# Optimization experiments

Measured on AMD Instinct MI355X. Metric: run time of the kernel, lower is better.

Reference implementation:

```python
import jax, jax.numpy as jnp
import numpy as np
import math

BLOCK_SIZE = 128  # config.block_size


def setup_inputs() -> dict:
    key = jax.random.key(0)
    k1, k2, k3 = jax.random.split(key, 3)
    B, H, S, D = 2, 12, 4096, 64
    return {
        "query_layer": jax.random.normal(k1, (B, H, S, D), dtype=jnp.float32),
        "key_layer": jax.random.normal(k2, (B, H, S, D), dtype=jnp.float32),
        "value_layer": jax.random.normal(k3, (B, H, S, D), dtype=jnp.float32),
        "attention_mask": jnp.zeros((B, 1, 1, S), dtype=jnp.float32),
    }


def reference(query_layer, key_layer, value_layer, attention_mask):
    d = query_layer.shape[-1]
    # [B,H,S,S] attention scores
    scores = jnp.einsum("bhqd,bhkd->bhqk", query_layer, key_layer) / math.sqrt(d)
    scores = scores + attention_mask
    # Faithful to source: the bottom-right block is OVERWRITTEN with
    # tril(ones, -1).T * finfo.min  (0 on/below diag, min strictly above)
    bs = BLOCK_SIZE
    causal_mask = jnp.tril(jnp.ones((bs, bs), dtype=scores.dtype), k=-1).T
    causal_mask = causal_mask * jnp.finfo(scores.dtype).min
    scores = scores.at[..., -bs:, -bs:].set(causal_mask)
    probs = jax.nn.softmax(scores, axis=-1)
    # dropout is identity in eval mode
    return jnp.einsum("bhqk,bhkd->bhqd", probs, value_layer)
```

## Files before the change

kernel.cpp:

```cpp
#include <hip/hip_runtime.h>

#define S_LEN 4096
#define DH    64
#define BQ    128
#define BK    64
#define NTILE (S_LEN / BK)
#define QBLKS (S_LEN / BQ)
#define NBH   24
#define NHEADS 12

typedef __attribute__((ext_vector_type(8))) short short8;
typedef __attribute__((ext_vector_type(4))) short short4v;
typedef __attribute__((ext_vector_type(4))) float f32x4;

#define PSTR 72
#define KSTR 72
#define VSTR 72
#define LOG2E 1.44269504088896f
#define MCONST (-12.99718425f)

#define NKCH (NBH * S_LEN * DH / 8)

__device__ __forceinline__ short f2bf(float x) {
    unsigned u = __builtin_bit_cast(unsigned, x);
    return (short)((u + 0x8000u) >> 16);
}

typedef __attribute__((address_space(1))) const unsigned int guint;
typedef __attribute__((address_space(3))) unsigned int luint;
__device__ __forceinline__ void g2l16(const short* g, short* l) {
    __builtin_amdgcn_global_load_lds((guint*)g, (luint*)l, 16, 0, 0);
}

__global__ __launch_bounds__(256)
void prepass(const float* __restrict__ K, const float* __restrict__ V,
             const float* __restrict__ M, short* __restrict__ Kf,
             short* __restrict__ Vtf, float* __restrict__ Mf)
{
    __shared__ __align__(16) short K_lds[BK * KSTR];
    __shared__ __align__(16) short Vt_lds[DH * VSTR];

    const int tid = threadIdx.x;
    const int bh  = blockIdx.x >> 6;
    const int t   = blockIdx.x & 63;
    const size_t base = ((size_t)bh * S_LEN + (size_t)t * BK) * DH;

    #pragma unroll
    for (int it = 0; it < 4; ++it) {
        int idx = tid + 256 * it;
        int row = idx >> 4, c4 = idx & 15;
        float4 v = *(const float4*)(K + base + (size_t)row * DH + 4 * c4);
        short4v b4 = { f2bf(v.x), f2bf(v.y), f2bf(v.z), f2bf(v.w) };
        *(short4v*)&K_lds[row * KSTR + 4 * c4] = b4;
    }
    {
        int kb = tid >> 4, db = tid & 15;
        const float* vp = V + base + (size_t)(4 * kb) * DH + 4 * db;
        float4 r0 = *(const float4*)(vp);
        float4 r1 = *(const float4*)(vp + DH);
        float4 r2 = *(const float4*)(vp + 2 * DH);
        float4 r3 = *(const float4*)(vp + 3 * DH);
        short4v c0 = { f2bf(r0.x), f2bf(r1.x), f2bf(r2.x), f2bf(r3.x) };
        short4v c1 = { f2bf(r0.y), f2bf(r1.y), f2bf(r2.y), f2bf(r3.y) };
        short4v c2 = { f2bf(r0.z), f2bf(r1.z), f2bf(r2.z), f2bf(r3.z) };
        short4v c3 = { f2bf(r0.w), f2bf(r1.w), f2bf(r2.w), f2bf(r3.w) };
        *(short4v*)&Vt_lds[(4 * db + 0) * VSTR + 4 * kb] = c0;
        *(short4v*)&Vt_lds[(4 * db + 1) * VSTR + 4 * kb] = c1;
        *(short4v*)&Vt_lds[(4 * db + 2) * VSTR + 4 * kb] = c2;
        *(short4v*)&Vt_lds[(4 * db + 3) * VSTR + 4 * kb] = c3;
    }
    __syncthreads();

    const size_t obase = (size_t)(bh * NTILE + t) * 4096;
    #pragma unroll
    for (int e = 0; e < 2; ++e) {
        int ci = tid + 256 * e;
        int lane = ci & 63, n = lane & 15, q = lane >> 4;
        {
            int kt = (ci >> 6) & 1, mt = ci >> 7;
            short8 f = *(const short8*)&K_lds[(16 * mt + n) * KSTR + 32 * kt + 8 * q];
            *(short8*)&Kf[obase + (size_t)ci * 8] = f;
        }
        {
            int d = (ci >> 6) & 3, kt2 = (ci >> 8) & 1;
            short8 g2 = *(const short8*)&Vt_lds[(16 * d + n) * VSTR + 32 * kt2 + 8 * q];
            *(short8*)&Vtf[obase + (size_t)ci * 8] = g2;
        }
    }
    if ((bh % NHEADS) == 0 && tid < 16) {
        int b_idx = bh / NHEADS;
        float4 mv = *(const float4*)(M + (size_t)b_idx * S_LEN + t * BK + 4 * tid);
        mv.x = mv.x * LOG2E + MCONST;
        mv.y = mv.y * LOG2E + MCONST;
        mv.z = mv.z * LOG2E + MCONST;
        mv.w = mv.w * LOG2E + MCONST;
        *(float4*)&Mf[(size_t)b_idx * S_LEN + t * BK + 4 * tid] = mv;
    }
}

__global__ __launch_bounds__(256, 3)
void fa6(const float* __restrict__ Q, const short* __restrict__ Kf,
         const short* __restrict__ Vtf, const float* __restrict__ Mf,
         float* __restrict__ O)
{
    __shared__ __align__(16) short Ks[2][4096];
    __shared__ __align__(16) short Vs[2][4096];
    __shared__ __align__(16) short P_lds[BQ * PSTR];

    const int tid  = threadIdx.x;
    const int w    = tid >> 6;
    const int lane = tid & 63;
    const int n    = lane & 15;
    const int quad = lane >> 4;

    const int bid  = blockIdx.x;
    const int x    = bid & 7;
    const int g    = bid >> 3;
    const int bh   = x + 8 * (g >> 5);
    const int qblk = g & 31;
    const bool special = (qblk == QBLKS - 1);

    const size_t base  = (size_t)bh * S_LEN * DH;
    const int    b_idx = bh / NHEADS;

    const float QSCALE = 0.125f * LOG2E;
    const int q0 = qblk * BQ + w * 32;
    short8 qf[2][2];
    #pragma unroll
    for (int s = 0; s < 2; ++s) {
        const float* qp = Q + base + (size_t)(q0 + 16 * s + n) * DH;
        #pragma unroll
        for (int kt = 0; kt < 2; ++kt) {
            const float* p = qp + 32 * kt + 8 * quad;
            float4 a = *(const float4*)p;
            float4 b = *(const float4*)(p + 4);
            short8 f;
            f[0] = f2bf(a.x * QSCALE); f[1] = f2bf(a.y * QSCALE);
            f[2] = f2bf(a.z * QSCALE); f[3] = f2bf(a.w * QSCALE);
            f[4] = f2bf(b.x * QSCALE); f[5] = f2bf(b.y * QSCALE);
            f[6] = f2bf(b.z * QSCALE); f[7] = f2bf(b.w * QSCALE);
            qf[s][kt] = f;
        }
    }

    f32x4 o[4][2];
    #pragma unroll
    for (int d = 0; d < 4; ++d)
        #pragma unroll
        for (int s = 0; s < 2; ++s) o[d][s] = (f32x4){0.f, 0.f, 0.f, 0.f};
    f32x4 lsum[2] = { (f32x4){0.f,0.f,0.f,0.f}, (f32x4){0.f,0.f,0.f,0.f} };

    const short8 ONES = { 0x3F80, 0x3F80, 0x3F80, 0x3F80,
                          0x3F80, 0x3F80, 0x3F80, 0x3F80 };
    const float* mrow = Mf + (size_t)b_idx * S_LEN;
    const short* Kg = Kf  + (size_t)(bh * NTILE) * 4096;
    const short* Vg = Vtf + (size_t)(bh * NTILE) * 4096;

    #pragma unroll
    for (int i = 0; i < 2; ++i) {
        int c = 2 * w + i;
        g2l16(Kg + c * 512 + lane * 8, &Ks[0][c * 512]);
        g2l16(Vg + c * 512 + lane * 8, &Vs[0][c * 512]);
    }
    __syncthreads();

    for (int t = 0; t < NTILE; ++t) {
        const bool sp = special && t >= NTILE - 2;
        const int  cur = t & 1, nxt = cur ^ 1;

        {
            int tn = (t + 1 < NTILE) ? t + 1 : t;
            const short* kg = Kg + (size_t)tn * 4096;
            const short* vg = Vg + (size_t)tn * 4096;
            #pragma unroll
            for (int i = 0; i < 2; ++i) {
                int c = 2 * w + i;
                g2l16(kg + c * 512 + lane * 8, &Ks[nxt][c * 512]);
                g2l16(vg + c * 512 + lane * 8, &Vs[nxt][c * 512]);
            }
        }

        if (!sp) {
            f32x4 acc[4][2];
            #pragma unroll
            for (int mt = 0; mt < 4; ++mt) {
                short8 k0 = *(const short8*)&Ks[cur][(2 * mt    ) * 512 + lane * 8];
                short8 k1 = *(const short8*)&Ks[cur][(2 * mt + 1) * 512 + lane * 8];
                f32x4 mk = *(const f32x4*)(mrow + t * BK + 16 * mt + 4 * quad);
                #pragma unroll
                for (int s = 0; s < 2; ++s) {
                    f32x4 c = mk;
                    c = __builtin_amdgcn_mfma_f32_16x16x32_bf16(k0, qf[s][0], c, 0, 0, 0);
                    c = __builtin_amdgcn_mfma_f32_16x16x32_bf16(k1, qf[s][1], c, 0, 0, 0);
                    acc[mt][s] = c;
                }
            }
            #pragma unroll
            for (int s = 0; s < 2; ++s) {
                int qrow = w * 32 + 16 * s + n;
                #pragma unroll
                for (int mt = 0; mt < 4; ++mt) {
                    float p0 = __builtin_amdgcn_exp2f(acc[mt][s][0]);
                    float p1 = __builtin_amdgcn_exp2f(acc[mt][s][1]);
                    float p2 = __builtin_amdgcn_exp2f(acc[mt][s][2]);
                    float p3 = __builtin_amdgcn_exp2f(acc[mt][s][3]);
                    unsigned d0 = __builtin_amdgcn_perm(
                        __builtin_bit_cast(unsigned, p1),
                        __builtin_bit_cast(unsigned, p0), 0x07060302u);
                    unsigned d1 = __builtin_amdgcn_perm(
                        __builtin_bit_cast(unsigned, p3),
                        __builtin_bit_cast(unsigned, p2), 0x07060302u);
                    *(uint2*)&P_lds[qrow * PSTR + 16 * mt + 4 * quad] = make_uint2(d0, d1);
                }
            }
        } else {
            #pragma unroll
            for (int s = 0; s < 2; ++s) {
                int ql2 = w * 32 + 16 * s + n;
                #pragma unroll
                for (int mt = 0; mt < 4; ++mt) {
                    int k0 = (t - (NTILE - 2)) * BK + 16 * mt + 4 * quad;
                    unsigned d0 = (k0     > ql2 ? 0u : 0x3900u)
                                | (k0 + 1 > ql2 ? 0u : 0x39000000u);
                    unsigned d1 = (k0 + 2 > ql2 ? 0u : 0x3900u)
                                | (k0 + 3 > ql2 ? 0u : 0x39000000u);
                    *(uint2*)&P_lds[ql2 * PSTR + 16 * mt + 4 * quad] = make_uint2(d0, d1);
                }
            }
        }

        #pragma unroll
        for (int kt2 = 0; kt2 < 2; ++kt2) {
            short8 pf0 = *(const short8*)&P_lds[(w * 32 + n) * PSTR + 32 * kt2 + 8 * quad];
            short8 pf1 = *(const short8*)&P_lds[(w * 32 + 16 + n) * PSTR + 32 * kt2 + 8 * quad];
            lsum[0] = __builtin_amdgcn_mfma_f32_16x16x32_bf16(ONES, pf0, lsum[0], 0, 0, 0);
            lsum[1] = __builtin_amdgcn_mfma_f32_16x16x32_bf16(ONES, pf1, lsum[1], 0, 0, 0);
            #pragma unroll
            for (int d = 0; d < 4; ++d) {
                short8 vf = *(const short8*)&Vs[cur][(kt2 * 4 + d) * 512 + lane * 8];
                o[d][0] = __builtin_amdgcn_mfma_f32_16x16x32_bf16(vf, pf0, o[d][0], 0, 0, 0);
                o[d][1] = __builtin_amdgcn_mfma_f32_16x16x32_bf16(vf, pf1, o[d][1], 0, 0, 0);
            }
        }

        __syncthreads();
    }

    #pragma unroll
    for (int s = 0; s < 2; ++s) {
        float inv = 1.0f / lsum[s][0];
        int qg = q0 + 16 * s + n;
        float* op = O + base + (size_t)qg * DH;
        #pragma unroll
        for (int d = 0; d < 4; ++d) {
            f32x4 r = o[d][s] * inv;
            *(f32x4*)(op + 16 * d + 4 * quad) = r;
        }
    }
}

extern "C" void kernel_launch(void* const* d_in, const int* in_sizes, int n_in,
                              void* d_out, int out_size, void* d_ws, size_t ws_size,
                              hipStream_t stream) {
    const float* Q = (const float*)d_in[0];
    const float* K = (const float*)d_in[1];
    const float* V = (const float*)d_in[2];
    const float* M = (const float*)d_in[3];
    float* O = (float*)d_out;

    short* Kf  = (short*)d_ws;
    short* Vtf = Kf + (size_t)NKCH * 8;
    float* Mf  = (float*)(Vtf + (size_t)NKCH * 8);

    prepass<<<dim3(NBH * NTILE), dim3(256), 0, stream>>>(K, V, M, Kf, Vtf, Mf);
    fa6<<<dim3(NBH * QBLKS), dim3(256), 0, stream>>>(Q, Kf, Vtf, Mf, O);
}
```

Baseline: 228.8 us.

## Load V fragments directly to registers and use per-wave P layout

V tiles are no longer staged through double-buffered LDS. Each lane now loads its V MFMA fragments from global memory straight into registers at the start of every tile. The P scratch is reorganised into a per-wave layout with 16-byte writes and a permuted read pattern, and the special causal tile now builds P directly in registers instead of writing it to LDS. This cuts LDS footprint and traffic, but adds global-load latency to every tile that is not prefetched ahead and raises register pressure.

```diff
diff --git a/kernel.cpp b/kernel.cpp
--- a/kernel.cpp
+++ b/kernel.cpp
@@ -12,13 +12,18 @@
 typedef __attribute__((ext_vector_type(8))) short short8;
 typedef __attribute__((ext_vector_type(4))) short short4v;
 typedef __attribute__((ext_vector_type(4))) float f32x4;
-
-#define PSTR 72
+typedef __attribute__((ext_vector_type(4))) unsigned uint4v;
+
 #define KSTR 72
 #define VSTR 72
 #define LOG2E 1.44269504088896f
 #define MCONST (-12.99718425f)
 
+#define P_MT    8
+#define P_NSTR  48
+#define P_QSTR  784
+#define P_SSTR  (4 * P_QSTR)
+#define P_WAVE  (2 * P_SSTR)
 #define NKCH (NBH * S_LEN * DH / 8)
 
 __device__ __forceinline__ short f2bf(float x) {
@@ -99,13 +104,12 @@
 }
 
 __global__ __launch_bounds__(256, 3)
-void fa6(const float* __restrict__ Q, const short* __restrict__ Kf,
+void fa7(const float* __restrict__ Q, const short* __restrict__ Kf,
          const short* __restrict__ Vtf, const float* __restrict__ Mf,
          float* __restrict__ O)
 {
     __shared__ __align__(16) short Ks[2][4096];
-    __shared__ __align__(16) short Vs[2][4096];
-    __shared__ __align__(16) short P_lds[BQ * PSTR];
+    __shared__ __align__(16) char  P_s[4 * P_WAVE];
 
     const int tid  = threadIdx.x;
     const int w    = tid >> 6;
@@ -154,13 +158,13 @@
                           0x3F80, 0x3F80, 0x3F80, 0x3F80 };
     const float* mrow = Mf + (size_t)b_idx * S_LEN;
     const short* Kg = Kf  + (size_t)(bh * NTILE) * 4096;
-    const short* Vg = Vtf + (size_t)(bh * NTILE) * 4096;
+    const short* Vg = Vtf + (size_t)(bh * NTILE) * 4096 + (size_t)lane * 8;
+    char* Pw = &P_s[w * P_WAVE];
 
     #pragma unroll
     for (int i = 0; i < 2; ++i) {
         int c = 2 * w + i;
         g2l16(Kg + c * 512 + lane * 8, &Ks[0][c * 512]);
-        g2l16(Vg + c * 512 + lane * 8, &Vs[0][c * 512]);
     }
     __syncthreads();
 
@@ -168,15 +172,20 @@
         const bool sp = special && t >= NTILE - 2;
         const int  cur = t & 1, nxt = cur ^ 1;
 
+        short8 vfr[8];
+        {
+            const short* vb = Vg + (size_t)t * 4096;
+            #pragma unroll
+            for (int i = 0; i < 8; ++i) vfr[i] = *(const short8*)(vb + i * 512);
+        }
+
         {
             int tn = (t + 1 < NTILE) ? t + 1 : t;
             const short* kg = Kg + (size_t)tn * 4096;
-            const short* vg = Vg + (size_t)tn * 4096;
             #pragma unroll
             for (int i = 0; i < 2; ++i) {
                 int c = 2 * w + i;
                 g2l16(kg + c * 512 + lane * 8, &Ks[nxt][c * 512]);
-                g2l16(vg + c * 512 + lane * 8, &Vs[nxt][c * 512]);
             }
         }
 
@@ -197,49 +206,53 @@
             }
             #pragma unroll
             for (int s = 0; s < 2; ++s) {
-                int qrow = w * 32 + 16 * s + n;
+                unsigned dd0[4], dd1[4];
                 #pragma unroll
                 for (int mt = 0; mt < 4; ++mt) {
                     float p0 = __builtin_amdgcn_exp2f(acc[mt][s][0]);
                     float p1 = __builtin_amdgcn_exp2f(acc[mt][s][1]);
                     float p2 = __builtin_amdgcn_exp2f(acc[mt][s][2]);
                     float p3 = __builtin_amdgcn_exp2f(acc[mt][s][3]);
-                    unsigned d0 = __builtin_amdgcn_perm(
+                    dd0[mt] = __builtin_amdgcn_perm(
                         __builtin_bit_cast(unsigned, p1),
                         __builtin_bit_cast(unsigned, p0), 0x07060302u);
-                    unsigned d1 = __builtin_amdgcn_perm(
+                    dd1[mt] = __builtin_amdgcn_perm(
                         __builtin_bit_cast(unsigned, p3),
                         __builtin_bit_cast(unsigned, p2), 0x07060302u);
-                    *(uint2*)&P_lds[qrow * PSTR + 16 * mt + 4 * quad] = make_uint2(d0, d1);
                 }
-            }
-        } else {
+                char* pw = Pw + s * P_SSTR + quad * P_QSTR + n * P_NSTR;
+                uint4v w0 = { dd0[0], dd1[0], dd0[1], dd1[1] };
+                uint4v w1 = { dd0[2], dd1[2], dd0[3], dd1[3] };
+                *(uint4v*)(pw)      = w0;
+                *(uint4v*)(pw + 16) = w1;
+            }
+        }
+
+        #pragma unroll
+        for (int kt2 = 0; kt2 < 2; ++kt2) {
+            const int mt = 2 * kt2 + (quad >> 1);
+            const int qa = (2 * quad) & 3;
+            const int qb = (2 * quad + 1) & 3;
             #pragma unroll
             for (int s = 0; s < 2; ++s) {
-                int ql2 = w * 32 + 16 * s + n;
+                short8 pf;
+                if (!sp) {
+                    const char* pb = Pw + s * P_SSTR + n * P_NSTR + mt * P_MT;
+                    uint2 lo = *(const uint2*)(pb + qa * P_QSTR);
+                    uint2 hi = *(const uint2*)(pb + qb * P_QSTR);
+                    uint4v u = { lo.x, lo.y, hi.x, hi.y };
+                    pf = __builtin_bit_cast(short8, u);
+                } else {
+                    int kb = (t - (NTILE - 2)) * BK + 32 * kt2 + 8 * quad;
+                    int ql = w * 32 + 16 * s + n;
+                    #pragma unroll
+                    for (int j = 0; j < 8; ++j)
+                        pf[j] = (kb + j > ql) ? (short)0 : (short)0x3900;
+                }
+                lsum[s] = __builtin_amdgcn_mfma_f32_16x16x32_bf16(ONES, pf, lsum[s], 0, 0, 0);
                 #pragma unroll
-                for (int mt = 0; mt < 4; ++mt) {
-                    int k0 = (t - (NTILE - 2)) * BK + 16 * mt + 4 * quad;
-                    unsigned d0 = (k0     > ql2 ? 0u : 0x3900u)
-                                | (k0 + 1 > ql2 ? 0u : 0x39000000u);
-                    unsigned d1 = (k0 + 2 > ql2 ? 0u : 0x3900u)
-                                | (k0 + 3 > ql2 ? 0u : 0x39000000u);
-                    *(uint2*)&P_lds[ql2 * PSTR + 16 * mt + 4 * quad] = make_uint2(d0, d1);
-                }
-            }
-        }
-
-        #pragma unroll
-        for (int kt2 = 0; kt2 < 2; ++kt2) {
-            short8 pf0 = *(const short8*)&P_lds[(w * 32 + n) * PSTR + 32 * kt2 + 8 * quad];
-            short8 pf1 = *(const short8*)&P_lds[(w * 32 + 16 + n) * PSTR + 32 * kt2 + 8 * quad];
-            lsum[0] = __builtin_amdgcn_mfma_f32_16x16x32_bf16(ONES, pf0, lsum[0], 0, 0, 0);
-            lsum[1] = __builtin_amdgcn_mfma_f32_16x16x32_bf16(ONES, pf1, lsum[1], 0, 0, 0);
-            #pragma unroll
-            for (int d = 0; d < 4; ++d) {
-                short8 vf = *(const short8*)&Vs[cur][(kt2 * 4 + d) * 512 + lane * 8];
-                o[d][0] = __builtin_amdgcn_mfma_f32_16x16x32_bf16(vf, pf0, o[d][0], 0, 0, 0);
-                o[d][1] = __builtin_amdgcn_mfma_f32_16x16x32_bf16(vf, pf1, o[d][1], 0, 0, 0);
+                for (int d = 0; d < 4; ++d)
+                    o[d][s] = __builtin_amdgcn_mfma_f32_16x16x32_bf16(vfr[kt2 * 4 + d], pf, o[d][s], 0, 0, 0);
             }
         }
 
@@ -273,5 +286,5 @@
     float* Mf  = (float*)(Vtf + (size_t)NKCH * 8);
 
     prepass<<<dim3(NBH * NTILE), dim3(256), 0, stream>>>(K, V, M, Kf, Vtf, Mf);
-    fa6<<<dim3(NBH * QBLKS), dim3(256), 0, stream>>>(Q, Kf, Vtf, Mf, O);
-}
+    fa7<<<dim3(NBH * QBLKS), dim3(256), 0, stream>>>(Q, Kf, Vtf, Mf, O);
+}
```

Measured after the change: 236.5 us. +3.4%, slower.
